# Kernel tuning notes

Hardware: AMD Instinct MI355X
Metric: run time of the kernel (lower is better)

Reference implementation:

```python
import jax, jax.numpy as jnp
import numpy as np

EPS = 1e-5

def setup_inputs() -> dict:
    key = jax.random.key(0)
    ks = jax.random.split(key, 6)
    C, r = 64, 4
    x = jax.random.normal(ks[0], (2, C, 16, 16, 16), dtype=jnp.float32)
    # ConvTranspose3d(C, C, kernel=r, stride=r, groups=C): weight [C, 1, r, r, r] -> squeeze to [C, r, r, r]
    w_ct = jax.random.normal(ks[1], (C, r, r, r), dtype=jnp.float32) * (1.0 / np.sqrt(r**3))
    b_ct = jax.random.normal(ks[2], (C,), dtype=jnp.float32) * 0.02
    # GroupNorm(num_groups=1) affine params
    gamma = jnp.ones((C,), dtype=jnp.float32)
    beta = jnp.zeros((C,), dtype=jnp.float32)
    # Conv3d(C, C, kernel=1, bias=False): weight [C, C, 1, 1, 1] -> [C_out, C_in]
    w_pw = jax.random.normal(ks[3], (C, C), dtype=jnp.float32) * (1.0 / np.sqrt(C))
    return {"x": x, "w_ct": w_ct, "b_ct": b_ct, "gamma": gamma, "beta": beta, "w_pw": w_pw}

def reference(x, w_ct, b_ct, gamma, beta, w_pw):
    N, C, D, H, W = x.shape
    r = w_ct.shape[-1]
    # Depthwise ConvTranspose3d with kernel==stride: non-overlapping scatter-multiply.
    # out[n,c,d*r+i,h*r+j,w*r+k] = x[n,c,d,h,w] * w_ct[c,i,j,k] + b_ct[c]
    y = jnp.einsum('ncdhw,cijk->ncdihjwk', x, w_ct).reshape(N, C, D * r, H * r, W * r)
    y = y + b_ct[None, :, None, None, None]
    # GroupNorm(num_groups=1): normalize over (C, D, H, W) per sample, per-channel affine.
    mean = jnp.mean(y, axis=(1, 2, 3, 4), keepdims=True)
    var = jnp.mean(jnp.square(y - mean), axis=(1, 2, 3, 4), keepdims=True)
    yn = (y - mean) * jax.lax.rsqrt(var + EPS)
    yn = yn * gamma[None, :, None, None, None] + beta[None, :, None, None, None]
    # Pointwise 1x1x1 conv (no bias): channel-mixing GEMM.
    out = jnp.einsum('ncdhw,oc->nodhw', yn, w_pw)
    return out
```

## Files before the change

kernel.cpp:

```cpp
#include <hip/hip_runtime.h>

typedef unsigned short u16;
typedef __attribute__((ext_vector_type(8))) short s16x8;
typedef __attribute__((ext_vector_type(4))) float f32x4;

__device__ __forceinline__ u16 f2bf(float f) {
    unsigned u = __builtin_bit_cast(unsigned, f);
    u += 0x7fffu + ((u >> 16) & 1u);
    return (u16)(u >> 16);
}

#define WS_SX   0
#define WS_SX2  128
#define WS_A    256
#define WS_K    8448

__global__ __launch_bounds__(256) void k_reduce(const float* __restrict__ x,
                                                float* __restrict__ ws) {
    int nc = blockIdx.x;
    const f32x4* p = (const f32x4*)(x + (size_t)nc * 4096);
    int t = threadIdx.x;
    float s = 0.f, s2 = 0.f;
    for (int it = 0; it < 4; ++it) {
        f32x4 v = p[t + it * 256];
        for (int e = 0; e < 4; ++e) { s += v[e]; s2 += v[e] * v[e]; }
    }
    for (int off = 32; off; off >>= 1) {
        s  += __shfl_down(s, off);
        s2 += __shfl_down(s2, off);
    }
    __shared__ float rs[4], rs2[4];
    int lane = t & 63, wv = t >> 6;
    if (lane == 0) { rs[wv] = s; rs2[wv] = s2; }
    __syncthreads();
    if (t == 0) {
        ws[WS_SX  + nc] = rs[0] + rs[1] + rs[2] + rs[3];
        ws[WS_SX2 + nc] = rs2[0] + rs2[1] + rs2[2] + rs2[3];
    }
}

__global__ __launch_bounds__(256) void k_stats(const float* __restrict__ w_ct,
                                               const float* __restrict__ b_ct,
                                               const float* __restrict__ gamma,
                                               const float* __restrict__ beta,
                                               const float* __restrict__ w_pw,
                                               float* __restrict__ ws) {
    __shared__ float s_sw[64], s_sw2[64], s_b[64], s_g[64], s_be[64];
    __shared__ float s_wpw[4096];
    __shared__ float s_mean[2], s_inv[2];
    int t = threadIdx.x;
    if (t < 64) {
        int c = t;
        float sw = 0.f, sw2 = 0.f;
        for (int q = 0; q < 64; ++q) {
            float w = w_ct[c * 64 + q];
            sw += w; sw2 += w * w;
        }
        s_sw[c] = sw; s_sw2[c] = sw2;
        s_b[c] = b_ct[c]; s_g[c] = gamma[c]; s_be[c] = beta[c];
    }
    for (int idx = t; idx < 4096; idx += 256) s_wpw[idx] = w_pw[idx];
    __syncthreads();
    if (t < 64) {
        int c = t;
        for (int n = 0; n < 2; ++n) {
            float sx  = ws[WS_SX  + n * 64 + c];
            float sx2 = ws[WS_SX2 + n * 64 + c];
            float ty  = s_sw[c]  * sx  + 262144.f * s_b[c];
            float ty2 = s_sw2[c] * sx2 + 2.f * s_b[c] * s_sw[c] * sx
                        + 262144.f * s_b[c] * s_b[c];
            for (int off = 32; off; off >>= 1) {
                ty  += __shfl_down(ty, off);
                ty2 += __shfl_down(ty2, off);
            }
            if (t == 0) {
                float mean = ty * (1.f / 16777216.f);
                float var  = ty2 * (1.f / 16777216.f) - mean * mean;
                s_mean[n] = mean;
                s_inv[n]  = rsqrtf(var + 1e-5f);
            }
        }
    }
    __syncthreads();
    for (int n = 0; n < 2; ++n) {
        float inv = s_inv[n];
        for (int idx = t; idx < 4096; idx += 256) {
            int c = idx & 63;
            ws[WS_A + n * 4096 + idx] = s_wpw[idx] * s_g[c] * inv;
        }
    }
    if (t < 128) {
        int n = t >> 6, o = t & 63;
        float inv = s_inv[n], mean = s_mean[n], k = 0.f;
        for (int c = 0; c < 64; ++c) {
            float scale = s_g[c] * inv;
            float shift = s_be[c] - mean * scale;
            k += s_wpw[o * 64 + c] * (s_b[c] * scale + shift);
        }
        ws[WS_K + t] = k;
    }
}

__global__ __launch_bounds__(256) void k_main(const float* __restrict__ x,
                                              const float* __restrict__ w_ct,
                                              const float* __restrict__ ws,
                                              float* __restrict__ out) {
    __shared__ __align__(16) float sW[64 * 64];
    __shared__ __align__(16) float sX[16 * 64];
    __shared__ __align__(16) float sA[64 * 68];
    __shared__ float sK[64];

    int t = threadIdx.x;
    int b = blockIdx.x;
    int n = b >> 8, d = (b >> 4) & 15, h = b & 15;

    const float* Aws = ws + WS_A + n * 4096;
    for (int idx = t; idx < 4096; idx += 256)
        sA[(idx >> 6) * 68 + (idx & 63)] = Aws[idx];
    if (t < 64) sK[t] = ws[WS_K + n * 64 + t];

    if (t < 64) {
        int c = t;
        const f32x4* wp = (const f32x4*)(w_ct + c * 64);
        for (int r = 0; r < 16; ++r) {
            f32x4 v = wp[r];
            for (int e = 0; e < 4; ++e) sW[(r * 4 + e) * 64 + c] = v[e];
        }
        const f32x4* xp = (const f32x4*)(x + ((size_t)n * 64 + c) * 4096 + d * 256 + h * 16);
        for (int r = 0; r < 4; ++r) {
            f32x4 v = xp[r];
            for (int e = 0; e < 4; ++e) sX[(r * 4 + e) * 64 + c] = v[e];
        }
    }
    __syncthreads();

    int lane = t & 63;
    int wid  = t >> 6;
    int colq = lane & 15;
    int quad = lane >> 4;

    s16x8 afrag[4][2];
    for (int mt = 0; mt < 4; ++mt) {
        int o = mt * 16 + colq;
        for (int kt = 0; kt < 2; ++kt) {
            int c0 = kt * 32 + quad * 8;
            const float* ap = &sA[o * 68 + c0];
            f32x4 f0 = *(const f32x4*)ap;
            f32x4 f1 = *(const f32x4*)(ap + 4);
            s16x8 fr;
            fr[0] = (short)f2bf(f0[0]); fr[1] = (short)f2bf(f0[1]);
            fr[2] = (short)f2bf(f0[2]); fr[3] = (short)f2bf(f0[3]);
            fr[4] = (short)f2bf(f1[0]); fr[5] = (short)f2bf(f1[1]);
            fr[6] = (short)f2bf(f1[2]); fr[7] = (short)f2bf(f1[3]);
            afrag[mt][kt] = fr;
        }
    }
    f32x4 kinit[4];
    for (int mt = 0; mt < 4; ++mt) {
        float kv = sK[mt * 16 + colq];
        kinit[mt][0] = kv; kinit[mt][1] = kv; kinit[mt][2] = kv; kinit[mt][3] = kv;
    }

    size_t base_n = (size_t)n << 24;
    for (int nt = 0; nt < 16; ++nt) {
        int q0   = wid * 256 + nt * 16;
        int ij   = q0 >> 6;
        int Wb   = q0 & 63;
        int Woff = Wb + colq;
        int wi   = Woff >> 2;
        int kf   = Woff & 3;
        int ijk  = ij * 4 + kf;

        s16x8 bfrag[2];
        for (int kt = 0; kt < 2; ++kt) {
            int c0 = kt * 32 + quad * 8;
            const float* wpp = &sW[ijk * 64 + c0];
            const float* xpp = &sX[wi  * 64 + c0];
            f32x4 w0 = *(const f32x4*)wpp, w1 = *(const f32x4*)(wpp + 4);
            f32x4 x0 = *(const f32x4*)xpp, x1 = *(const f32x4*)(xpp + 4);
            s16x8 fr;
            fr[0] = (short)f2bf(w0[0] * x0[0]); fr[1] = (short)f2bf(w0[1] * x0[1]);
            fr[2] = (short)f2bf(w0[2] * x0[2]); fr[3] = (short)f2bf(w0[3] * x0[3]);
            fr[4] = (short)f2bf(w1[0] * x1[0]); fr[5] = (short)f2bf(w1[1] * x1[1]);
            fr[6] = (short)f2bf(w1[2] * x1[2]); fr[7] = (short)f2bf(w1[3] * x1[3]);
            bfrag[kt] = fr;
        }

        int i_f = ij >> 2, j_f = ij & 3;
        size_t sp = (size_t)((4 * d + i_f) * 4096 + (4 * h + j_f) * 64 + Wb + quad * 4);
        for (int mt = 0; mt < 4; ++mt) {
            f32x4 acc = kinit[mt];
            acc = __builtin_amdgcn_mfma_f32_16x16x32_bf16(bfrag[0], afrag[mt][0], acc, 0, 0, 0);
            acc = __builtin_amdgcn_mfma_f32_16x16x32_bf16(bfrag[1], afrag[mt][1], acc, 0, 0, 0);
            int o = mt * 16 + colq;
            float* op = out + base_n + ((size_t)o << 18) + sp;
            *(f32x4*)op = acc;
        }
    }
}

extern "C" void kernel_launch(void* const* d_in, const int* in_sizes, int n_in,
                              void* d_out, int out_size, void* d_ws, size_t ws_size,
                              hipStream_t stream) {
    const float* x     = (const float*)d_in[0];
    const float* w_ct  = (const float*)d_in[1];
    const float* b_ct  = (const float*)d_in[2];
    const float* gamma = (const float*)d_in[3];
    const float* beta  = (const float*)d_in[4];
    const float* w_pw  = (const float*)d_in[5];
    float* ws  = (float*)d_ws;
    float* out = (float*)d_out;

    k_reduce<<<128, 256, 0, stream>>>(x, ws);
    k_stats<<<1, 256, 0, stream>>>(w_ct, b_ct, gamma, beta, w_pw, ws);
    k_main<<<512, 256, 0, stream>>>(x, w_ct, ws, out);
}
```

Measured before the change: 172.1 us.

## Fuse stats kernel into main kernel, store bf16 operands in LDS, nontemporal stores

Removes the single-block k_stats launch. Each main block now recomputes the GroupNorm mean/inv and the folded A matrix and bias vector itself, which drops one launch and the serial one-block stage between kernels. The w_ct and x tiles are staged in LDS as bf16 with padded stride, halving LDS reads in the inner loop. Output stores are made nontemporal. In exchange every block redundantly reads w_pw and w_ct and does extra prologue work, and x and w are rounded to bf16 before multiplying, which adds a small precision loss.

Measured after the change: 170.3 us. About the same (-1.0%).

```diff
diff --git a/kernel.cpp b/kernel.cpp
--- a/kernel.cpp
+++ b/kernel.cpp
@@ -3,17 +3,22 @@
 typedef unsigned short u16;
 typedef __attribute__((ext_vector_type(8))) short s16x8;
 typedef __attribute__((ext_vector_type(4))) float f32x4;
+typedef __attribute__((ext_vector_type(4))) unsigned int u32x4;
 
 __device__ __forceinline__ u16 f2bf(float f) {
     unsigned u = __builtin_bit_cast(unsigned, f);
     u += 0x7fffu + ((u >> 16) & 1u);
     return (u16)(u >> 16);
 }
+__device__ __forceinline__ float lo_bf(unsigned v) {
+    return __builtin_bit_cast(float, v << 16);
+}
+__device__ __forceinline__ float hi_bf(unsigned v) {
+    return __builtin_bit_cast(float, v & 0xffff0000u);
+}
 
 #define WS_SX   0
 #define WS_SX2  128
-#define WS_A    256
-#define WS_K    8448
 
 __global__ __launch_bounds__(256) void k_reduce(const float* __restrict__ x,
                                                 float* __restrict__ ws) {
@@ -39,98 +44,92 @@
     }
 }
 
-__global__ __launch_bounds__(256) void k_stats(const float* __restrict__ w_ct,
-                                               const float* __restrict__ b_ct,
-                                               const float* __restrict__ gamma,
-                                               const float* __restrict__ beta,
-                                               const float* __restrict__ w_pw,
-                                               float* __restrict__ ws) {
-    __shared__ float s_sw[64], s_sw2[64], s_b[64], s_g[64], s_be[64];
-    __shared__ float s_wpw[4096];
-    __shared__ float s_mean[2], s_inv[2];
-    int t = threadIdx.x;
-    if (t < 64) {
-        int c = t;
-        float sw = 0.f, sw2 = 0.f;
-        for (int q = 0; q < 64; ++q) {
-            float w = w_ct[c * 64 + q];
-            sw += w; sw2 += w * w;
-        }
-        s_sw[c] = sw; s_sw2[c] = sw2;
-        s_b[c] = b_ct[c]; s_g[c] = gamma[c]; s_be[c] = beta[c];
-    }
-    for (int idx = t; idx < 4096; idx += 256) s_wpw[idx] = w_pw[idx];
-    __syncthreads();
-    if (t < 64) {
-        int c = t;
-        for (int n = 0; n < 2; ++n) {
-            float sx  = ws[WS_SX  + n * 64 + c];
-            float sx2 = ws[WS_SX2 + n * 64 + c];
-            float ty  = s_sw[c]  * sx  + 262144.f * s_b[c];
-            float ty2 = s_sw2[c] * sx2 + 2.f * s_b[c] * s_sw[c] * sx
-                        + 262144.f * s_b[c] * s_b[c];
-            for (int off = 32; off; off >>= 1) {
-                ty  += __shfl_down(ty, off);
-                ty2 += __shfl_down(ty2, off);
-            }
-            if (t == 0) {
-                float mean = ty * (1.f / 16777216.f);
-                float var  = ty2 * (1.f / 16777216.f) - mean * mean;
-                s_mean[n] = mean;
-                s_inv[n]  = rsqrtf(var + 1e-5f);
-            }
-        }
-    }
-    __syncthreads();
-    for (int n = 0; n < 2; ++n) {
-        float inv = s_inv[n];
-        for (int idx = t; idx < 4096; idx += 256) {
-            int c = idx & 63;
-            ws[WS_A + n * 4096 + idx] = s_wpw[idx] * s_g[c] * inv;
-        }
-    }
-    if (t < 128) {
-        int n = t >> 6, o = t & 63;
-        float inv = s_inv[n], mean = s_mean[n], k = 0.f;
-        for (int c = 0; c < 64; ++c) {
-            float scale = s_g[c] * inv;
-            float shift = s_be[c] - mean * scale;
-            k += s_wpw[o * 64 + c] * (s_b[c] * scale + shift);
-        }
-        ws[WS_K + t] = k;
-    }
-}
-
+#define SWS 96
 __global__ __launch_bounds__(256) void k_main(const float* __restrict__ x,
                                               const float* __restrict__ w_ct,
+                                              const float* __restrict__ b_ct,
+                                              const float* __restrict__ gamma,
+                                              const float* __restrict__ beta,
+                                              const float* __restrict__ w_pw,
                                               const float* __restrict__ ws,
                                               float* __restrict__ out) {
-    __shared__ __align__(16) float sW[64 * 64];
-    __shared__ __align__(16) float sX[16 * 64];
+    __shared__ __align__(16) u16   sWb[64 * SWS];
+    __shared__ __align__(16) u16   sXb[16 * SWS];
     __shared__ __align__(16) float sA[64 * 68];
     __shared__ float sK[64];
+    __shared__ float p_sw[256], p_sw2[256];
+    __shared__ float s_b[64], s_g[64], s_be[64];
+    __shared__ float s_mi[2];
 
     int t = threadIdx.x;
     int b = blockIdx.x;
     int n = b >> 8, d = (b >> 4) & 15, h = b & 15;
 
-    const float* Aws = ws + WS_A + n * 4096;
-    for (int idx = t; idx < 4096; idx += 256)
-        sA[(idx >> 6) * 68 + (idx & 63)] = Aws[idx];
-    if (t < 64) sK[t] = ws[WS_K + n * 64 + t];
-
+    {
+        int c = t & 63, qr = t >> 6;
+        const f32x4* wp = (const f32x4*)(w_ct + c * 64 + qr * 16);
+        float sw = 0.f, sw2 = 0.f;
+        for (int r = 0; r < 4; ++r) {
+            f32x4 v = wp[r];
+            for (int e = 0; e < 4; ++e) {
+                float f = v[e];
+                sw += f; sw2 += f * f;
+                sWb[(qr * 16 + r * 4 + e) * SWS + c] = f2bf(f);
+            }
+        }
+        p_sw[t] = sw; p_sw2[t] = sw2;
+    }
     if (t < 64) {
         int c = t;
-        const f32x4* wp = (const f32x4*)(w_ct + c * 64);
-        for (int r = 0; r < 16; ++r) {
-            f32x4 v = wp[r];
-            for (int e = 0; e < 4; ++e) sW[(r * 4 + e) * 64 + c] = v[e];
-        }
         const f32x4* xp = (const f32x4*)(x + ((size_t)n * 64 + c) * 4096 + d * 256 + h * 16);
         for (int r = 0; r < 4; ++r) {
             f32x4 v = xp[r];
-            for (int e = 0; e < 4; ++e) sX[(r * 4 + e) * 64 + c] = v[e];
-        }
+            for (int e = 0; e < 4; ++e) sXb[(r * 4 + e) * SWS + c] = f2bf(v[e]);
+        }
+        s_b[c] = b_ct[c]; s_g[c] = gamma[c]; s_be[c] = beta[c];
+    }
+    __syncthreads();
+
+    if (t < 64) {
+        int c = t;
+        float sw  = p_sw[c]  + p_sw[64 + c]  + p_sw[128 + c]  + p_sw[192 + c];
+        float sw2 = p_sw2[c] + p_sw2[64 + c] + p_sw2[128 + c] + p_sw2[192 + c];
+        float sx  = ws[WS_SX  + n * 64 + c];
+        float sx2 = ws[WS_SX2 + n * 64 + c];
+        float bc  = s_b[c];
+        float ty  = sw  * sx  + 262144.f * bc;
+        float ty2 = sw2 * sx2 + 2.f * bc * sw * sx + 262144.f * bc * bc;
+        for (int off = 32; off; off >>= 1) {
+            ty  += __shfl_down(ty, off);
+            ty2 += __shfl_down(ty2, off);
+        }
+        if (t == 0) {
+            float mean = ty * (1.f / 16777216.f);
+            float var  = ty2 * (1.f / 16777216.f) - mean * mean;
+            s_mi[0] = mean;
+            s_mi[1] = rsqrtf(var + 1e-5f);
+        }
+    }
+    __syncthreads();
+
+    float mean = s_mi[0], inv = s_mi[1];
+    for (int k = 0; k < 16; ++k) {
+        int idx = t + k * 256;
+        int c = idx & 63;
+        sA[(idx >> 6) * 68 + c] = w_pw[idx] * s_g[c] * inv;
+    }
+    if (t < 64) {
+        int o = t;
+        const f32x4* wp = (const f32x4*)(w_pw + o * 64);
+        float k = 0.f;
+        for (int r = 0; r < 16; ++r) {
+            f32x4 v = wp[r];
+            for (int e = 0; e < 4; ++e) {
+                int c = r * 4 + e;
+                k += v[e] * (s_g[c] * inv * (s_b[c] - mean) + s_be[c]);
+            }
+        }
+        sK[o] = k;
     }
     __syncthreads();
 
@@ -174,15 +173,15 @@
         s16x8 bfrag[2];
         for (int kt = 0; kt < 2; ++kt) {
             int c0 = kt * 32 + quad * 8;
-            const float* wpp = &sW[ijk * 64 + c0];
-            const float* xpp = &sX[wi  * 64 + c0];
-            f32x4 w0 = *(const f32x4*)wpp, w1 = *(const f32x4*)(wpp + 4);
-            f32x4 x0 = *(const f32x4*)xpp, x1 = *(const f32x4*)(xpp + 4);
+            u32x4 wv = *(const u32x4*)&sWb[ijk * SWS + c0];
+            u32x4 xv = *(const u32x4*)&sXb[wi  * SWS + c0];
             s16x8 fr;
-            fr[0] = (short)f2bf(w0[0] * x0[0]); fr[1] = (short)f2bf(w0[1] * x0[1]);
-            fr[2] = (short)f2bf(w0[2] * x0[2]); fr[3] = (short)f2bf(w0[3] * x0[3]);
-            fr[4] = (short)f2bf(w1[0] * x1[0]); fr[5] = (short)f2bf(w1[1] * x1[1]);
-            fr[6] = (short)f2bf(w1[2] * x1[2]); fr[7] = (short)f2bf(w1[3] * x1[3]);
+            for (int e = 0; e < 4; ++e) {
+                float pl = lo_bf(wv[e]) * lo_bf(xv[e]);
+                float ph = hi_bf(wv[e]) * hi_bf(xv[e]);
+                fr[2 * e]     = (short)f2bf(pl);
+                fr[2 * e + 1] = (short)f2bf(ph);
+            }
             bfrag[kt] = fr;
         }
 
@@ -194,7 +193,7 @@
             acc = __builtin_amdgcn_mfma_f32_16x16x32_bf16(bfrag[1], afrag[mt][1], acc, 0, 0, 0);
             int o = mt * 16 + colq;
             float* op = out + base_n + ((size_t)o << 18) + sp;
-            *(f32x4*)op = acc;
+            __builtin_nontemporal_store(acc, (f32x4*)op);
         }
     }
 }
@@ -212,6 +211,5 @@
     float* out = (float*)d_out;
 
     k_reduce<<<128, 256, 0, stream>>>(x, ws);
-    k_stats<<<1, 256, 0, stream>>>(w_ct, b_ct, gamma, beta, w_pw, ws);
-    k_main<<<512, 256, 0, stream>>>(x, w_ct, ws, out);
-}
+    k_main<<<512, 256, 0, stream>>>(x, w_ct, b_ct, gamma, beta, w_pw, ws, out);
+}
```
